# Optimization experiments

Hardware: AMD Instinct MI355X
Metric: run time of the kernel (lower is better)

## Reference

```python
import jax, jax.numpy as jnp
import numpy as np

B, T, D, H, O = 512, 256, 128, 256, 128

def _lin(x, W, b):
    # torch Linear: y = x @ W.T + b, W is [out, in]
    return x @ W.T + b

def _n2n(x):
    return jnp.nan_to_num(x, nan=0.0, posinf=0.0, neginf=0.0)

def _forward(x, x_mask, x_delta, noise,
             W_emb, b_emb, W_d1, b_d1, W_d2, b_d2, W_c, b_c,
             W_z, b_z, W_r, b_r, W_h, b_h, ln_g, ln_b, W_o, b_o):
    # input embedding
    x = _n2n(_lin(x, W_emb, b_emb))                       # [B,T,D]
    x_mean = jax.lax.stop_gradient(jnp.mean(x, axis=1))   # [B,D] (detach in torch)
    x_mean = _n2n(x_mean)
    # deltas, clamped (vectorized over T; decay MLP has no recurrence)
    d = jnp.clip(jnp.nan_to_num(x_delta, nan=0.0, posinf=100.0, neginf=0.0), 0.0, 100.0)
    gamma_x = jax.nn.sigmoid(_lin(jax.nn.relu(_lin(d, W_d1, b_d1)), W_d2, b_d2))  # [B,T,D]
    m = x_mask
    x_hat = m * x + (1.0 - m) * (gamma_x * x_mean[:, None, :])
    conf = jax.nn.sigmoid(_lin(jnp.concatenate([x_hat, d], axis=-1), W_c, b_c))   # [B,T,D]
    x_final = _n2n(x_hat * conf + noise * (1.0 - conf))
    # concat [x_final, m, d] is the time-varying part of gate inputs; nan_to_num
    xc = _n2n(jnp.concatenate([x_final, m, d], axis=-1))  # [B,T,3D]
    D3 = 3 * D
    # split gate weights into input-part and hidden-part; precompute input GEMMs
    zx = jnp.einsum('btk,hk->bth', xc, W_z[:, :D3]) + b_z  # [B,T,H]
    rx = jnp.einsum('btk,hk->bth', xc, W_r[:, :D3]) + b_r
    hx = jnp.einsum('btk,hk->bth', xc, W_h[:, :D3]) + b_h
    W_zh, W_rh, W_hh = W_z[:, D3:], W_r[:, D3:], W_h[:, D3:]

    def step(h, inp):
        zx_t, rx_t, hx_t = inp
        z = jax.nn.sigmoid(zx_t + h @ W_zh.T)
        r = jax.nn.sigmoid(rx_t + h @ W_rh.T)
        h_tilde = jnp.tanh(hx_t + (r * h) @ W_hh.T)
        h = _n2n((1.0 - z) * h + z * h_tilde)
        return h, None

    h0 = jnp.zeros((x.shape[0], H), dtype=x.dtype)
    h_last, _ = jax.lax.scan(step, h0, (zx.swapaxes(0, 1), rx.swapaxes(0, 1), hx.swapaxes(0, 1)))
    h_last = _n2n(h_last)
    # output head: LayerNorm(eps=1e-5) -> Dropout(eval: identity) -> Linear
    mu = jnp.mean(h_last, axis=-1, keepdims=True)
    var = jnp.mean((h_last - mu) ** 2, axis=-1, keepdims=True)
    ln = (h_last - mu) / jnp.sqrt(var + 1e-5) * ln_g + ln_b
    return _lin(ln, W_o, b_o)


def setup_inputs() -> dict:
    key = jax.random.key(0)
    ks = jax.random.split(key, 24)
    def W(k, o, i):
        s = 1.0 / np.sqrt(i)
        return jax.random.uniform(k, (o, i), jnp.float32, -s, s)
    def bvec(k, o, i):
        s = 1.0 / np.sqrt(i)
        return jax.random.uniform(k, (o,), jnp.float32, -s, s)
    D3H = 3 * D + H
    return {
        'x': jax.random.normal(ks[0], (B, T, D), jnp.float32),
        'x_mask': (jax.random.uniform(ks[1], (B, T, D)) < 0.8).astype(jnp.float32),
        'x_delta': jax.random.uniform(ks[2], (B, T, D), jnp.float32, 0.0, 10.0),
        'noise': jax.random.normal(ks[3], (B, T, D), jnp.float32),
        'W_emb': W(ks[4], D, D), 'b_emb': bvec(ks[5], D, D),
        'W_d1': W(ks[6], D, D), 'b_d1': bvec(ks[7], D, D),
        'W_d2': W(ks[8], D, D), 'b_d2': bvec(ks[9], D, D),
        'W_c': W(ks[10], D, 2 * D), 'b_c': bvec(ks[11], D, 2 * D),
        'W_z': W(ks[12], H, D3H), 'b_z': bvec(ks[13], H, D3H),
        'W_r': W(ks[14], H, D3H), 'b_r': bvec(ks[15], H, D3H),
        'W_h': W(ks[16], H, D3H), 'b_h': bvec(ks[17], H, D3H),
        'ln_g': jnp.ones((H,), jnp.float32), 'ln_b': jnp.zeros((H,), jnp.float32),
        'W_o': W(ks[18], O, H), 'b_o': bvec(ks[19], O, H),
    }


def reference(x, x_mask, x_delta, noise, W_emb, b_emb, W_d1, b_d1, W_d2, b_d2,
              W_c, b_c, W_z, b_z, W_r, b_r, W_h, b_h, ln_g, ln_b, W_o, b_o):
    return _forward(x, x_mask, x_delta, noise, W_emb, b_emb, W_d1, b_d1, W_d2, b_d2,
                    W_c, b_c, W_z, b_z, W_r, b_r, W_h, b_h, ln_g, ln_b, W_o, b_o)
```

## Files before the change

kernel.cpp:

```cpp
#include <hip/hip_runtime.h>
#include <hip/hip_fp16.h>
#include <math.h>

#define BB 512
#define TT 256
#define DD 128
#define HH 256
#define OO 128
#define KH 640
#define BT (BB*TT)

typedef unsigned int uint_t;
typedef _Float16 f16x8 __attribute__((ext_vector_type(8)));
typedef float f32x4 __attribute__((ext_vector_type(4)));

__device__ __forceinline__ float sigmoidf_(float x){ return 1.0f/(1.0f+__expf(-x)); }
__device__ __forceinline__ float tanhf_(float x){ float e = __expf(-2.0f*x); return 2.0f/(1.0f+e) - 1.0f; }
__device__ __forceinline__ float clipd_(float x){ return fminf(fmaxf(x, 0.f), 100.f); }

typedef _Float16 h2v __attribute__((ext_vector_type(2)));
__device__ __forceinline__ float d2(uint_t a, uint_t b, float c){
#if __has_builtin(__builtin_amdgcn_fdot2)
    return __builtin_amdgcn_fdot2(__builtin_bit_cast(h2v, a), __builtin_bit_cast(h2v, b), c, false);
#else
    __half2 ha = __builtin_bit_cast(__half2, a);
    __half2 hb = __builtin_bit_cast(__half2, b);
    return c + __half2float(ha.x)*__half2float(hb.x) + __half2float(ha.y)*__half2float(hb.y);
#endif
}
__device__ __forceinline__ uint_t pack2(float a, float b){
    __half2 h; h.x = __float2half(a); h.y = __float2half(b);
    return __builtin_bit_cast(uint_t, h);
}

static const size_t SZ_XC   = (size_t)BT*384*2;
static const size_t TAIL_SZ = 589824 + 393216 + 3072 + 262144 + 524288 + 32768*3 + 65536;

__global__ __launch_bounds__(128) void k_wprep(const float* __restrict__ Wz, const float* __restrict__ Wr,
                                               const float* __restrict__ Wh, const float* __restrict__ bz,
                                               const float* __restrict__ br, const float* __restrict__ bh,
                                               __half* __restrict__ Wcat, __half* __restrict__ Wrec,
                                               float* __restrict__ bcat){
    int gj = blockIdx.x; int j = gj & 255;
    const float* src  = (gj < 256 ? Wz : (gj < 512 ? Wr : Wh)) + (size_t)j*KH;
    const float* bsrc = (gj < 256 ? bz : (gj < 512 ? br : bh));
    for(int k=threadIdx.x; k<384; k+=128) Wcat[(size_t)gj*384 + k] = __float2half(src[k]);
    for(int k=threadIdx.x; k<256; k+=128) Wrec[(size_t)gj*256 + k] = __float2half(src[384+k]);
    if(threadIdx.x==0) bcat[gj] = bsrc[j];
}

__global__ __launch_bounds__(256) void k_cvt(const float* __restrict__ a, const float* __restrict__ b,
                                             const float* __restrict__ c, const float* __restrict__ d,
                                             __half* __restrict__ oa, __half* __restrict__ ob,
                                             __half* __restrict__ oc, __half* __restrict__ od){
    int i = blockIdx.x*256 + threadIdx.x;
    if(i < 16384){
        oa[i] = __float2half(a[i]);
        ob[i] = __float2half(b[i]);
        oc[i] = __float2half(c[i]);
    }
    od[i] = __float2half(d[i]);
}

__global__ __launch_bounds__(256,4) void k_embm(const float* __restrict__ x,
                                                const __half* __restrict__ Wh,
                                                const float* __restrict__ bias,
                                                __half* __restrict__ xc){
    __shared__ __align__(16) uint4 TxU[128*16];
    const int tid = threadIdx.x;
    const long row0 = (long)blockIdx.x*128;
    {
        const int srow = tid>>1, shalf = tid&1;
        const long gr = row0 + srow;
        const float4* gx = (const float4*)(x + gr*DD + shalf*64);
        #pragma unroll
        for(int u=0;u<8;++u){
            float4 a = gx[u*2], q = gx[u*2+1];
            uint4 pk;
            pk.x = pack2(a.x,a.y); pk.y = pack2(a.z,a.w);
            pk.z = pack2(q.x,q.y); pk.w = pack2(q.z,q.w);
            int unit = shalf*8 + u;
            TxU[srow*16 + (unit ^ (srow&7))] = pk;
        }
    }
    __syncthreads();
    const int wv = tid>>6, lane = tid&63, g = lane>>4, r16 = lane&15;
    const int wrow0 = wv*32;
    const uint4* WU = (const uint4*)Wh;
    f32x4 acc[2][8];
    #pragma unroll
    for(int i=0;i<2;++i)
        #pragma unroll
        for(int jj=0;jj<8;++jj) acc[i][jj] = (f32x4){0.f,0.f,0.f,0.f};
    #pragma unroll
    for(int ks=0;ks<4;++ks){
        f16x8 af[2], bf[8];
        #pragma unroll
        for(int mf=0;mf<2;++mf){
            int rr = wrow0 + mf*16 + r16;
            af[mf] = __builtin_bit_cast(f16x8, TxU[rr*16 + ((ks*4+g) ^ (rr&7))]);
        }
        #pragma unroll
        for(int nf=0;nf<8;++nf){
            int col = nf*16 + r16;
            bf[nf] = __builtin_bit_cast(f16x8, WU[col*16 + ks*4 + g]);
        }
        #pragma unroll
        for(int mf=0;mf<2;++mf)
            #pragma unroll
            for(int nf=0;nf<8;++nf)
                acc[mf][nf] = __builtin_amdgcn_mfma_f32_16x16x32_f16(af[mf], bf[nf], acc[mf][nf], 0,0,0);
    }
// ... 43 lines not shown
    const float* __restrict__ noise,
    const __half* __restrict__ Wd1h, const float* __restrict__ bd1,
    const __half* __restrict__ Wd2h, const float* __restrict__ bd2,
    const __half* __restrict__ Wch,  const float* __restrict__ bc,
    const float* __restrict__ xmean){
    __shared__ __align__(16) uint4 TdU[128*16];
    __shared__ __align__(16) uint4 TtU[128*16];
    __half* Tth = (__half*)TtU;
    const int tid = threadIdx.x;
    const long row0 = (long)blockIdx.x*128;
    const int b = (int)(row0 >> 8);

    {
        const int srow = tid>>1, shalf = tid&1;
        const long gr = row0 + srow;
        const float4* gd = (const float4*)(xdelta + gr*DD + shalf*64);
        const float4* gm = (const float4*)(xmask  + gr*DD + shalf*64);
        uint4* xcu = (uint4*)(xc + gr*384);
        #pragma unroll
        for(int u=0;u<8;++u){
            float4 a = gd[u*2], q = gd[u*2+1];
            uint4 pk;
            pk.x = pack2(clipd_(a.x), clipd_(a.y));
            pk.y = pack2(clipd_(a.z), clipd_(a.w));
            pk.z = pack2(clipd_(q.x), clipd_(q.y));
            pk.w = pack2(clipd_(q.z), clipd_(q.w));
            int unit = shalf*8 + u;
            TdU[srow*16 + (unit ^ (srow&7))] = pk;
            xcu[32 + unit] = pk;
        }
        #pragma unroll
        for(int u=0;u<8;++u){
            float4 a = gm[u*2], q = gm[u*2+1];
            uint4 pk;
            pk.x = pack2(a.x,a.y); pk.y = pack2(a.z,a.w);
            pk.z = pack2(q.x,q.y); pk.w = pack2(q.z,q.w);
            xcu[16 + shalf*8 + u] = pk;
        }
    }
    __syncthreads();

    const int wv = tid>>6, lane = tid&63, g = lane>>4, r16 = lane&15;
    const int wrow0 = wv*32;
    const uint4* W1U = (const uint4*)Wd1h;
    const uint4* W2U = (const uint4*)Wd2h;
    const uint4* WcU = (const uint4*)Wch;
    f32x4 acc[2][8];

    #pragma unroll
    for(int i=0;i<2;++i)
        #pragma unroll
        for(int jj=0;jj<8;++jj) acc[i][jj] = (f32x4){0.f,0.f,0.f,0.f};
    #pragma unroll
    for(int ks=0;ks<4;++ks){
        f16x8 af[2], bf[8];
        #pragma unroll
        for(int mf=0;mf<2;++mf){
            int rr = wrow0 + mf*16 + r16;
            af[mf] = __builtin_bit_cast(f16x8, TdU[rr*16 + ((ks*4+g) ^ (rr&7))]);
        }
        #pragma unroll
        for(int nf=0;nf<8;++nf){
            int col = nf*16 + r16;
            bf[nf] = __builtin_bit_cast(f16x8, W1U[col*16 + ks*4 + g]);
        }
        #pragma unroll
        for(int mf=0;mf<2;++mf)
            #pragma unroll
            for(int nf=0;nf<8;++nf)
                acc[mf][nf] = __builtin_amdgcn_mfma_f32_16x16x32_f16(af[mf], bf[nf], acc[mf][nf], 0,0,0);
    }
    #pragma unroll
    for(int nf=0;nf<8;++nf){
        int col = nf*16 + r16;
        float bb = bd1[col];
        int u = col>>3, cl = col&7;
        #pragma unroll
        for(int mf=0;mf<2;++mf){
            int rowb = wrow0 + mf*16 + g*4;
            f32x4 v = acc[mf][nf];
            #pragma unroll
            for(int e=0;e<4;++e){
                int rr = rowb + e;
                float t = v[e] + bb; t = t > 0.f ? t : 0.f;
                Tth[(rr*16 + (u ^ (rr&7)))*8 + cl] = __float2half(t);
            }
        }
    }

    #pragma unroll
    for(int i=0;i<2;++i)
        #pragma unroll
        for(int jj=0;jj<8;++jj) acc[i][jj] = (f32x4){0.f,0.f,0.f,0.f};
    #pragma unroll
    for(int ks=0;ks<4;++ks){
        f16x8 af[2], bf[8];
        #pragma unroll
        for(int mf=0;mf<2;++mf){
            int rr = wrow0 + mf*16 + r16;
            af[mf] = __builtin_bit_cast(f16x8, TtU[rr*16 + ((ks*4+g) ^ (rr&7))]);
        }
        #pragma unroll
        for(int nf=0;nf<8;++nf){
            int col = nf*16 + r16;
            bf[nf] = __builtin_bit_cast(f16x8, W2U[col*16 + ks*4 + g]);
        }
        #pragma unroll
        for(int mf=0;mf<2;++mf)
            #pragma unroll
            for(int nf=0;nf<8;++nf)
                acc[mf][nf] = __builtin_amdgcn_mfma_f32_16x16x32_f16(af[mf], bf[nf], acc[mf][nf], 0,0,0);
    }

    #pragma unroll
    for(int nf=0;nf<8;++nf){
        int col = nf*16 + r16;
        float b2 = bd2[col];
        float xm = xmean[b*DD + col];
        int u = col>>3, cl = col&7;
        #pragma unroll
        for(int mf=0;mf<2;++mf){
            int rowb = wrow0 + mf*16 + g*4;
            f32x4 v = acc[mf][nf];
            #pragma unroll
            for(int e=0;e<4;++e){
                int rr = rowb + e;
                long grow = row0 + rr;
                float m  = xmask[grow*DD + col];
                float x1 = __half2float(xc[grow*384 + col]);
                float gmm = sigmoidf_(v[e] + b2);
                float xh = m*x1 + (1.f-m)*gmm*xm;
                Tth[(rr*16 + (u ^ (rr&7)))*8 + cl] = __float2half(xh);
            }
        }
    }

    #pragma unroll
    for(int i=0;i<2;++i)
        #pragma unroll
        for(int jj=0;jj<8;++jj) acc[i][jj] = (f32x4){0.f,0.f,0.f,0.f};
    #pragma unroll
    for(int ks=0;ks<4;++ks){
        f16x8 af[2], bf[8];
        #pragma unroll
        for(int mf=0;mf<2;++mf){
            int rr = wrow0 + mf*16 + r16;
            af[mf] = __builtin_bit_cast(f16x8, TtU[rr*16 + ((ks*4+g) ^ (rr&7))]);
        }
        #pragma unroll
        for(int nf=0;nf<8;++nf){
            int col = nf*16 + r16;
            bf[nf] = __builtin_bit_cast(f16x8, WcU[col*32 + ks*4 + g]);
        }
        #pragma unroll
        for(int mf=0;mf<2;++mf)
            #pragma unroll
            for(int nf=0;nf<8;++nf)
                acc[mf][nf] = __builtin_amdgcn_mfma_f32_16x16x32_f16(af[mf], bf[nf], acc[mf][nf], 0,0,0);
    }
    #pragma unroll
    for(int ks=0;ks<4;++ks){
        f16x8 af[2], bf[8];
        #pragma unroll
        for(int mf=0;mf<2;++mf){
            int rr = wrow0 + mf*16 + r16;
            af[mf] = __builtin_bit_cast(f16x8, TdU[rr*16 + ((ks*4+g) ^ (rr&7))]);
        }
        #pragma unroll
        for(int nf=0;nf<8;++nf){
            int col = nf*16 + r16;
            bf[nf] = __builtin_bit_cast(f16x8, WcU[col*32 + 16 + ks*4 + g]);
        }
        #pragma unroll
        for(int mf=0;mf<2;++mf)
            #pragma unroll
            for(int nf=0;nf<8;++nf)
                acc[mf][nf] = __builtin_amdgcn_mfma_f32_16x16x32_f16(af[mf], bf[nf], acc[mf][nf], 0,0,0);
    }

    #pragma unroll
    for(int nf=0;nf<8;++nf){
        int col = nf*16 + r16;
        float bcc = bc[col];
        int u = col>>3, cl = col&7;
        #pragma unroll
        for(int mf=0;mf<2;++mf){
            int rowb = wrow0 + mf*16 + g*4;
            f32x4 v = acc[mf][nf];
            #pragma unroll
            for(int e=0;e<4;++e){
                int rr = rowb + e;
                long grow = row0 + rr;
                float conf = sigmoidf_(v[e] + bcc);
                float xh = __half2float(Tth[(rr*16 + (u ^ (rr&7)))*8 + cl]);
                float nz = noise[grow*DD + col];
                xc[grow*384 + col] = __float2half(xh*conf + nz*(1.f-conf));
            }
        }
    }
}

__global__ __launch_bounds__(256) void k_projm(const __half* __restrict__ xc,
                                               const __half* __restrict__ Wcat,
                                               const float* __restrict__ bcat,
                                               __half* __restrict__ px,
                                               int lTc, int chunk){
    __shared__ __align__(16) __half As[128*64];
    __shared__ __align__(16) __half Bs[128*64];
    const int tid = threadIdx.x;
    const int rblk = blockIdx.x * 128;
    const int ct0  = blockIdx.y * 128;
    const int mTc = (1<<lTc) - 1;

    const int row = tid >> 1;
    const int hf  = tid & 1;
    const int ar  = rblk + row;
    const long grow = ((long)(ar >> lTc))*TT + ((long)chunk << lTc) + (ar & mTc);
    const uint4* gA = (const uint4*)(xc + grow*384);
    const uint4* gB = (const uint4*)(Wcat + (size_t)(ct0 + row)*384);
    uint4* AsU = (uint4*)As;
    uint4* BsU = (uint4*)Bs;

    const int wv = tid >> 6;
    const int wm = wv >> 1, wn = wv & 1;
    const int l  = tid & 63;
    const int g  = l >> 4, r16 = l & 15;

    f32x4 acc[4][4];
    #pragma unroll
    for(int i=0;i<4;++i)
        #pragma unroll
        for(int jj=0;jj<4;++jj) acc[i][jj] = (f32x4){0.f,0.f,0.f,0.f};

    for(int bk=0; bk<6; ++bk){
        uint4 av[4], bv[4];
        #pragma unroll
        for(int u=0;u<4;++u){ av[u] = gA[bk*8 + hf*4 + u]; bv[u] = gB[bk*8 + hf*4 + u]; }
        if(bk) __syncthreads();
        #pragma unroll
        for(int u=0;u<4;++u){
            int uu = hf*4 + u;
            AsU[row*8 + (uu ^ (row&7))] = av[u];
            BsU[row*8 + (uu ^ (row&7))] = bv[u];
        }
        __syncthreads();
        #pragma unroll
        for(int ks=0;ks<2;++ks){
            f16x8 af[4], bf[4];
            #pragma unroll
            for(int mf=0;mf<4;++mf){
                int rr = wm*64 + mf*16 + r16;
                af[mf] = __builtin_bit_cast(f16x8, AsU[rr*8 + ((ks*4+g) ^ (rr&7))]);
            }
            #pragma unroll
            for(int nf=0;nf<4;++nf){
                int rr = wn*64 + nf*16 + r16;
                bf[nf] = __builtin_bit_cast(f16x8, BsU[rr*8 + ((ks*4+g) ^ (rr&7))]);
            }
            #pragma unroll
            for(int mf=0;mf<4;++mf)
                #pragma unroll
                for(int nf=0;nf<4;++nf)
                    acc[mf][nf] = __builtin_amdgcn_mfma_f32_16x16x32_f16(af[mf], bf[nf], acc[mf][nf], 0,0,0);
        }
    }
    #pragma unroll
    for(int nf=0; nf<4; ++nf){
        int col = ct0 + wn*64 + nf*16 + r16;
        float bb = bcat[col];
        #pragma unroll
        for(int mf=0; mf<4; ++mf){
            int r0 = rblk + wm*64 + mf*16 + g*4;
            f32x4 v = acc[mf][nf];
            #pragma unroll
            for(int e=0;e<4;++e)
                px[(size_t)(r0+e)*768 + col] = __float2half(v[e] + bb);
        }
    }
}

__global__ __launch_bounds__(512,2) void k_gruc(const __half* __restrict__ pxc,
                                                const __half* __restrict__ Wrec,
                                                float* __restrict__ hstate,
                                                int Tc, int init){
    __shared__ __align__(16) __half h16[2][256];
    __shared__ __align__(16) __half rh16[2][256];
    __shared__ __align__(16) uint_t pxs[2][768];
    const int t  = threadIdx.x;
    const int j  = t >> 1;
    const int kh = t & 1;
    const long b0 = (long)blockIdx.x*2;
    const uint_t* Wr32 = (const uint_t*)Wrec;

    uint_t wz[64], wr[64], wh[64];
    #pragma unroll
    for(int q=0;q<64;++q){
        wz[q] = Wr32[(size_t)(      j)*128 + kh*64 + q];
        wr[q] = Wr32[(size_t)(256 + j)*128 + kh*64 + q];
        wh[q] = Wr32[(size_t)(512 + j)*128 + kh*64 + q];
    }

    const uint_t* px32 = (const uint_t*)pxc;
    auto ldpx = [&](int tl, int f)->uint_t{
        int row = (f >= 384); int off = f - row*384;
        return px32[((size_t)(b0+row)*Tc + tl)*384 + off];
    };

    float hreg0, hreg1;
    if(init){ hreg0 = 0.f; hreg1 = 0.f; }
    else    { hreg0 = hstate[(b0+0)*HH + j]; hreg1 = hstate[(b0+1)*HH + j]; }
    if(kh==0){ h16[0][j] = __float2half(hreg0); h16[1][j] = __float2half(hreg1); }
    pxs[0][t] = ldpx(0, t);
    if(t < 256) pxs[0][t+512] = ldpx(0, t+512);
    __syncthreads();

    const uint_t* h0p = ((const uint_t*)&h16[0][0]) + kh*64;
    const uint_t* h1p = ((const uint_t*)&h16[1][0]) + kh*64;
    const uint_t* r0p = ((const uint_t*)&rh16[0][0]) + kh*64;
    const uint_t* r1p = ((const uint_t*)&rh16[1][0]) + kh*64;

    for(int s=0; s<Tc; ++s){
        const int cur = s & 1;
        uint_t nf0 = 0, nf1 = 0;
        if(s < Tc-1){ nf0 = ldpx(s+1, t); if(t < 256) nf1 = ldpx(s+1, t+512); }

        const __half* pxcur = (const __half*)pxs[cur];
        float az0=0.f, az1=0.f, ar0=0.f, ar1=0.f;
        #pragma unroll
        for(int q=0;q<64;q+=4){
            uint4 hv0 = *(const uint4*)(h0p + q);
            uint4 hv1 = *(const uint4*)(h1p + q);
            az0=d2(wz[q+0],hv0.x,az0); ar0=d2(wr[q+0],hv0.x,ar0); az1=d2(wz[q+0],hv1.x,az1); ar1=d2(wr[q+0],hv1.x,ar1);
            az0=d2(wz[q+1],hv0.y,az0); ar0=d2(wr[q+1],hv0.y,ar0); az1=d2(wz[q+1],hv1.y,az1); ar1=d2(wr[q+1],hv1.y,ar1);
            az0=d2(wz[q+2],hv0.z,az0); ar0=d2(wr[q+2],hv0.z,ar0); az1=d2(wz[q+2],hv1.z,az1); ar1=d2(wr[q+2],hv1.z,ar1);
            az0=d2(wz[q+3],hv0.w,az0); ar0=d2(wr[q+3],hv0.w,ar0); az1=d2(wz[q+3],hv1.w,az1); ar1=d2(wr[q+3],hv1.w,ar1);
        }
        az0 += __shfl_xor(az0,1); az1 += __shfl_xor(az1,1);
        ar0 += __shfl_xor(ar0,1); ar1 += __shfl_xor(ar1,1);
        float z0 = sigmoidf_(__half2float(pxcur[        j]) + az0);
        float z1 = sigmoidf_(__half2float(pxcur[768   + j]) + az1);
        float r0 = sigmoidf_(__half2float(pxcur[256   + j]) + ar0);
        float r1 = sigmoidf_(__half2float(pxcur[768+256+j]) + ar1);
        if(kh==0){
            rh16[0][j] = __float2half(r0*hreg0);
            rh16[1][j] = __float2half(r1*hreg1);
        }
        __syncthreads();
        float ah0=0.f, ah1=0.f;
        #pragma unroll
        for(int q=0;q<64;q+=4){
            uint4 rv0 = *(const uint4*)(r0p + q);
            uint4 rv1 = *(const uint4*)(r1p + q);
            ah0=d2(wh[q+0],rv0.x,ah0); ah1=d2(wh[q+0],rv1.x,ah1);
            ah0=d2(wh[q+1],rv0.y,ah0); ah1=d2(wh[q+1],rv1.y,ah1);
            ah0=d2(wh[q+2],rv0.z,ah0); ah1=d2(wh[q+2],rv1.z,ah1);
            ah0=d2(wh[q+3],rv0.w,ah0); ah1=d2(wh[q+3],rv1.w,ah1);
        }
        ah0 += __shfl_xor(ah0,1); ah1 += __shfl_xor(ah1,1);
        float ht0 = tanhf_(__half2float(pxcur[512    + j]) + ah0);
        float ht1 = tanhf_(__half2float(pxcur[768+512+j]) + ah1);
        hreg0 = (1.f - z0)*hreg0 + z0*ht0;
        hreg1 = (1.f - z1)*hreg1 + z1*ht1;
        if(kh==0){
            h16[0][j] = __float2half(hreg0);
            h16[1][j] = __float2half(hreg1);
        }
        if(s < Tc-1){
            pxs[cur^1][t] = nf0;
            if(t < 256) pxs[cur^1][t+512] = nf1;
        }
        __syncthreads();
    }
    if(kh==0){
        hstate[(b0+0)*HH + j] = hreg0;
        hstate[(b0+1)*HH + j] = hreg1;
    }
}

__global__ __launch_bounds__(256) void k_lnout(const float* __restrict__ hbuf,
    const float* __restrict__ lng, const float* __restrict__ lnb,
    const float* __restrict__ Wo, const float* __restrict__ bo,
    float* __restrict__ out){
    __shared__ __align__(16) float ln_s[HH];
    __shared__ float red[8];
    const int b = blockIdx.x, j = threadIdx.x;
    const float v = hbuf[(long)b*HH + j];
    float s = v, ss = v*v;
    const int lane = j & 63, w = j >> 6;
    for(int off=32; off>0; off>>=1){
        s  += __shfl_down(s,  off);
        ss += __shfl_down(ss, off);
    }
    if(lane == 0){ red[w] = s; red[4+w] = ss; }
    __syncthreads();
    float tot  = red[0]+red[1]+red[2]+red[3];
    float tot2 = red[4]+red[5]+red[6]+red[7];
    float mu  = tot  * (1.0f/HH);
    float var = tot2 * (1.0f/HH) - mu*mu;
    float rstd = rsqrtf(var + 1e-5f);
    ln_s[j] = (v - mu)*rstd*lng[j] + lnb[j];
    __syncthreads();
    if(j < OO){
        float acc = bo[j];
        const float4* w4 = (const float4*)(Wo + j*HH);
        const float4* l4 = (const float4*)ln_s;
        for(int k4=0;k4<HH/4;++k4){
            float4 wv = w4[k4], c = l4[k4];
            acc += wv.x*c.x + wv.y*c.y + wv.z*c.z + wv.w*c.w;
        }
        out[(long)b*OO + j] = acc;
    }
}


__global__ __launch_bounds__(128) void k_emb_o(const float* __restrict__ x,
                                               const float* __restrict__ W,
                                               const float* __restrict__ bias,
                                               float* __restrict__ x1){
    __shared__ __align__(16) float xs[8][DD];
    const int j = threadIdx.x;
    const long row0 = (long)blockIdx.x * 32;
    const float bj = bias[j];
    const float4* W4 = (const float4*)(W + j*DD);
    for(int g=0; g<4; ++g){
        const long rbase = row0 + g*8;
        for(int r=0;r<8;++r) xs[r][j] = x[(rbase+r)*DD + j];
        __syncthreads();
        float acc[8];
        #pragma unroll
        for(int r=0;r<8;++r) acc[r] = bj;
        for(int k4=0;k4<DD/4;++k4){
            float4 w = W4[k4];
            #pragma unroll
            for(int r=0;r<8;++r){
                float4 c = ((const float4*)xs[r])[k4];
                acc[r] += c.x*w.x + c.y*w.y + c.z*w.z + c.w*w.w;
            }
        }
        for(int r=0;r<8;++r) x1[(rbase+r)*DD + j] = acc[r];
        __syncthreads();
    }
}

__global__ __launch_bounds__(128) void k_mean_o(const float* __restrict__ x1,
                                                float* __restrict__ xmean){
    const int j = threadIdx.x;
    const int b = blockIdx.x;
    const float* p = x1 + (long)b*TT*DD + j;
    float s = 0.f;
    for(int t=0;t<TT;++t) s += p[(long)t*DD];
    xmean[b*DD + j] = s * (1.0f/TT);
}

__global__ __launch_bounds__(128) void k_gate_o(float* __restrict__ xf,
    const float* __restrict__ xmask, const float* __restrict__ xdelta,
    const float* __restrict__ noise,
    const float* __restrict__ Wd1, const float* __restrict__ bd1,
    const float* __restrict__ Wd2, const float* __restrict__ bd2,
// ... 115 lines not shown
        float ah = bhj;
        for(int k4=0;k4<96;++k4){
            float4 wh = Wh4[k4];
            float4 v = cb[k4];
            ah += v.x*wh.x + v.y*wh.y + v.z*wh.z + v.w*wh.w;
        }
        const float4* rp = (const float4*)rh[bl];
        for(int k4=0;k4<64;++k4){
            float4 wh = Wh4[96 + k4];
            float4 v = rp[k4];
            ah += v.x*wh.x + v.y*wh.y + v.z*wh.z + v.w*wh.w;
        }
        float ht = tanhf(ah);
        float hold = xcs[bl][384 + j];
        float hn = (1.f - z)*hold + z*ht;
        xcs[bl][384 + j] = hn;
        __syncthreads();
    }
    hout[(bbase + bl)*HH + j] = xcs[bl][384 + j];
}


extern "C" void kernel_launch(void* const* d_in, const int* in_sizes, int n_in,
                              void* d_out, int out_size, void* d_ws, size_t ws_size,
                              hipStream_t stream){
    const float* x      = (const float*)d_in[0];
    const float* xmask  = (const float*)d_in[1];
    const float* xdelta = (const float*)d_in[2];
    const float* noise  = (const float*)d_in[3];
    const float* W_emb  = (const float*)d_in[4];
    const float* b_emb  = (const float*)d_in[5];
    const float* W_d1   = (const float*)d_in[6];
    const float* b_d1   = (const float*)d_in[7];
    const float* W_d2   = (const float*)d_in[8];
    const float* b_d2   = (const float*)d_in[9];
    const float* W_c    = (const float*)d_in[10];
    const float* b_c    = (const float*)d_in[11];
    const float* W_z    = (const float*)d_in[12];
    const float* b_z    = (const float*)d_in[13];
    const float* W_r    = (const float*)d_in[14];
    const float* b_r    = (const float*)d_in[15];
    const float* W_h    = (const float*)d_in[16];
    const float* b_h    = (const float*)d_in[17];
    const float* ln_g   = (const float*)d_in[18];
    const float* ln_b   = (const float*)d_in[19];
    const float* W_o    = (const float*)d_in[20];
    const float* b_o    = (const float*)d_in[21];
    float* out = (float*)d_out;
    char* ws = (char*)d_ws;

    int Tc = 0, lTc = 0;
    {
        const int cand[3]  = {128, 64, 32};
        const int lcand[3] = {7, 6, 5};
        for(int i=0;i<3;++i){
            size_t need = SZ_XC + (size_t)cand[i]*786432 + TAIL_SZ;
            if(ws_size >= need){ Tc = cand[i]; lTc = lcand[i]; break; }
        }
    }

    if(Tc > 0){
        __half* xc    = (__half*)(ws);
        char*   p     = ws + SZ_XC;
        __half* pxc   = (__half*)p;              p += (size_t)Tc*786432;
        __half* Wcat  = (__half*)p;              p += 589824;
        __half* Wrec  = (__half*)p;              p += 393216;
        float*  bcat  = (float*)p;               p += 3072;
        float*  xmean = (float*)p;               p += 262144;
        float*  hstate= (float*)p;               p += 524288;
        __half* Wembh = (__half*)p;              p += 32768;
        __half* Wd1h  = (__half*)p;              p += 32768;
        __half* Wd2h  = (__half*)p;              p += 32768;
        __half* Wch   = (__half*)p;

        k_wprep<<<dim3(768),   dim3(128), 0, stream>>>(W_z,W_r,W_h,b_z,b_r,b_h, Wcat, Wrec, bcat);
        k_cvt  <<<dim3(128),   dim3(256), 0, stream>>>(W_emb, W_d1, W_d2, W_c, Wembh, Wd1h, Wd2h, Wch);
        k_embm <<<dim3(BT/128),dim3(256), 0, stream>>>(x, Wembh, b_emb, xc);
        k_meanv<<<dim3(BB),    dim3(256), 0, stream>>>(xc, xmean);
        k_gatem<<<dim3(BT/128),dim3(256), 0, stream>>>(xc, xmask, xdelta, noise,
                                                       Wd1h,b_d1,Wd2h,b_d2,Wch,b_c, xmean);
        const int nchunk = TT / Tc;
        for(int c=0; c<nchunk; ++c){
            k_projm<<<dim3(BB*Tc/128, 6), dim3(256), 0, stream>>>(xc, Wcat, bcat, pxc, lTc, c);
            k_gruc <<<dim3(BB/2), dim3(512), 0, stream>>>(pxc, Wrec, hstate, Tc, c==0 ? 1 : 0);
        }
        k_lnout<<<dim3(BB), dim3(256), 0, stream>>>(hstate, ln_g, ln_b, W_o, b_o, out);
    } else {
        float* xf    = (float*)ws;
        float* xmean = (float*)(ws + (size_t)BT*DD*4);
        float* hbuf  = (float*)(ws + (size_t)BT*DD*4 + (size_t)BB*DD*4);
        k_emb_o  <<<dim3(BT/32), dim3(128), 0, stream>>>(x, W_emb, b_emb, xf);
        k_mean_o <<<dim3(BB),    dim3(128), 0, stream>>>(xf, xmean);
        k_gate_o <<<dim3(BT/32), dim3(128), 0, stream>>>(xf, xmask, xdelta, noise,
                                                         W_d1,b_d1,W_d2,b_d2,W_c,b_c, xmean);
        k_gru_o  <<<dim3(BB/4),  dim3(1024),0, stream>>>(xf, xmask, xdelta,
                                                         W_z,b_z,W_r,b_r,W_h,b_h, hbuf);
        k_lnout  <<<dim3(BB),    dim3(256), 0, stream>>>(hbuf, ln_g, ln_b, W_o, b_o, out);
    }
}
```

Baseline: 1.388 ms.

## Split GRU recurrent dot products four ways with padded LDS layout for h

Reworks the recurrent GRU kernel so each thread covers two hidden units across a quarter of the K dimension, instead of one unit across half of K. Weights are held in uint4 vectors and partial sums are reduced with two shuffle-xor steps. The fp16 hidden state in LDS gets a padded layout (72-word stride per 64 entries) so the four K-slices read from different banks. The intent is to cut LDS bank conflicts and load count per step, at the cost of extra shuffles and more accumulators.

```diff
diff --git a/kernel.cpp b/kernel.cpp
--- a/kernel.cpp
+++ b/kernel.cpp
@@ -237,8 +237,8 @@
             #pragma unroll
             for(int e=0;e<4;++e){
                 int rr = rowb + e;
-                float t = v[e] + bb; t = t > 0.f ? t : 0.f;
-                Tth[(rr*16 + (u ^ (rr&7)))*8 + cl] = __float2half(t);
+                float tt = v[e] + bb; tt = tt > 0.f ? tt : 0.f;
+                Tth[(rr*16 + (u ^ (rr&7)))*8 + cl] = __float2half(tt);
             }
         }
     }
@@ -438,21 +438,24 @@
                                                 const __half* __restrict__ Wrec,
                                                 float* __restrict__ hstate,
                                                 int Tc, int init){
-    __shared__ __align__(16) __half h16[2][256];
-    __shared__ __align__(16) __half rh16[2][256];
+    __shared__ __align__(16) uint_t hU[288];
+    __shared__ __align__(16) uint_t rhU[288];
     __shared__ __align__(16) uint_t pxs[2][768];
     const int t  = threadIdx.x;
-    const int j  = t >> 1;
-    const int kh = t & 1;
+    const int ks = t & 3;
+    const int jj = t >> 2;
     const long b0 = (long)blockIdx.x*2;
-    const uint_t* Wr32 = (const uint_t*)Wrec;
-
-    uint_t wz[64], wr[64], wh[64];
-    #pragma unroll
-    for(int q=0;q<64;++q){
-        wz[q] = Wr32[(size_t)(      j)*128 + kh*64 + q];
-        wr[q] = Wr32[(size_t)(256 + j)*128 + kh*64 + q];
-        wh[q] = Wr32[(size_t)(512 + j)*128 + kh*64 + q];
+    const uint4* Wr4 = (const uint4*)Wrec;
+
+    uint4 wz0[8], wz1[8], wr0[8], wr1[8], wh0[8], wh1[8];
+    #pragma unroll
+    for(int q=0;q<8;++q){
+        wz0[q] = Wr4[(size_t)(      jj     )*32 + ks*8 + q];
+        wz1[q] = Wr4[(size_t)(      jj+128 )*32 + ks*8 + q];
+        wr0[q] = Wr4[(size_t)(256 + jj     )*32 + ks*8 + q];
+        wr1[q] = Wr4[(size_t)(256 + jj+128 )*32 + ks*8 + q];
+        wh0[q] = Wr4[(size_t)(512 + jj     )*32 + ks*8 + q];
+        wh1[q] = Wr4[(size_t)(512 + jj+128 )*32 + ks*8 + q];
     }
 
     const uint_t* px32 = (const uint_t*)pxc;
@@ -461,18 +464,33 @@
         return px32[((size_t)(b0+row)*Tc + tl)*384 + off];
     };
 
-    float hreg0, hreg1;
-    if(init){ hreg0 = 0.f; hreg1 = 0.f; }
-    else    { hreg0 = hstate[(b0+0)*HH + j]; hreg1 = hstate[(b0+1)*HH + j]; }
-    if(kh==0){ h16[0][j] = __float2half(hreg0); h16[1][j] = __float2half(hreg1); }
+    const int ho0 = ((jj>>6)*72) + (jj&63);
+    const int ho1 = ho0 + 144;
+    __half* hh  = (__half*)hU;
+    __half* rhh = (__half*)rhU;
+
+    float h00,h01,h10,h11;
+    if(init){ h00=0.f; h01=0.f; h10=0.f; h11=0.f; }
+    else{
+        h00 = hstate[(b0+0)*HH + jj];
+        h01 = hstate[(b0+0)*HH + jj+128];
+        h10 = hstate[(b0+1)*HH + jj];
+        h11 = hstate[(b0+1)*HH + jj+128];
+    }
+    if(ks==0){
+        hh[      ho0] = __float2half(h00);
+        hh[      ho1] = __float2half(h01);
+        hh[288 + ho0] = __float2half(h10);
+        hh[288 + ho1] = __float2half(h11);
+    }
     pxs[0][t] = ldpx(0, t);
     if(t < 256) pxs[0][t+512] = ldpx(0, t+512);
     __syncthreads();
 
-    const uint_t* h0p = ((const uint_t*)&h16[0][0]) + kh*64;
-    const uint_t* h1p = ((const uint_t*)&h16[1][0]) + kh*64;
-    const uint_t* r0p = ((const uint_t*)&rh16[0][0]) + kh*64;
-    const uint_t* r1p = ((const uint_t*)&rh16[1][0]) + kh*64;
+    const uint4* h0p = ((const uint4*)hU)       + ks*9;
+    const uint4* h1p = ((const uint4*)hU)  + 36 + ks*9;
+    const uint4* r0p = ((const uint4*)rhU)      + ks*9;
+    const uint4* r1p = ((const uint4*)rhU) + 36 + ks*9;
 
     for(int s=0; s<Tc; ++s){
         const int cur = s & 1;
@@ -480,45 +498,74 @@
         if(s < Tc-1){ nf0 = ldpx(s+1, t); if(t < 256) nf1 = ldpx(s+1, t+512); }
 
         const __half* pxcur = (const __half*)pxs[cur];
-        float az0=0.f, az1=0.f, ar0=0.f, ar1=0.f;
-        #pragma unroll
-        for(int q=0;q<64;q+=4){
-            uint4 hv0 = *(const uint4*)(h0p + q);
-            uint4 hv1 = *(const uint4*)(h1p + q);
-            az0=d2(wz[q+0],hv0.x,az0); ar0=d2(wr[q+0],hv0.x,ar0); az1=d2(wz[q+0],hv1.x,az1); ar1=d2(wr[q+0],hv1.x,ar1);
-            az0=d2(wz[q+1],hv0.y,az0); ar0=d2(wr[q+1],hv0.y,ar0); az1=d2(wz[q+1],hv1.y,az1); ar1=d2(wr[q+1],hv1.y,ar1);
-            az0=d2(wz[q+2],hv0.z,az0); ar0=d2(wr[q+2],hv0.z,ar0); az1=d2(wz[q+2],hv1.z,az1); ar1=d2(wr[q+2],hv1.z,ar1);
-            az0=d2(wz[q+3],hv0.w,az0); ar0=d2(wr[q+3],hv0.w,ar0); az1=d2(wz[q+3],hv1.w,az1); ar1=d2(wr[q+3],hv1.w,ar1);
-        }
-        az0 += __shfl_xor(az0,1); az1 += __shfl_xor(az1,1);
-        ar0 += __shfl_xor(ar0,1); ar1 += __shfl_xor(ar1,1);
-        float z0 = sigmoidf_(__half2float(pxcur[        j]) + az0);
-        float z1 = sigmoidf_(__half2float(pxcur[768   + j]) + az1);
-        float r0 = sigmoidf_(__half2float(pxcur[256   + j]) + ar0);
-        float r1 = sigmoidf_(__half2float(pxcur[768+256+j]) + ar1);
-        if(kh==0){
-            rh16[0][j] = __float2half(r0*hreg0);
-            rh16[1][j] = __float2half(r1*hreg1);
-        }
-        __syncthreads();
-        float ah0=0.f, ah1=0.f;
-        #pragma unroll
-        for(int q=0;q<64;q+=4){
-            uint4 rv0 = *(const uint4*)(r0p + q);
-            uint4 rv1 = *(const uint4*)(r1p + q);
-            ah0=d2(wh[q+0],rv0.x,ah0); ah1=d2(wh[q+0],rv1.x,ah1);
-            ah0=d2(wh[q+1],rv0.y,ah0); ah1=d2(wh[q+1],rv1.y,ah1);
-            ah0=d2(wh[q+2],rv0.z,ah0); ah1=d2(wh[q+2],rv1.z,ah1);
-            ah0=d2(wh[q+3],rv0.w,ah0); ah1=d2(wh[q+3],rv1.w,ah1);
-        }
-        ah0 += __shfl_xor(ah0,1); ah1 += __shfl_xor(ah1,1);
-        float ht0 = tanhf_(__half2float(pxcur[512    + j]) + ah0);
-        float ht1 = tanhf_(__half2float(pxcur[768+512+j]) + ah1);
-        hreg0 = (1.f - z0)*hreg0 + z0*ht0;
-        hreg1 = (1.f - z1)*hreg1 + z1*ht1;
-        if(kh==0){
-            h16[0][j] = __float2half(hreg0);
-            h16[1][j] = __float2half(hreg1);
+        float az00=0.f,az01=0.f,az10=0.f,az11=0.f;
+        float ar00=0.f,ar01=0.f,ar10=0.f,ar11=0.f;
+        #pragma unroll
+        for(int it=0; it<8; ++it){
+            uint4 hv0 = h0p[it], hv1 = h1p[it];
+            uint4 a = wz0[it], b = wz1[it], c = wr0[it], d = wr1[it];
+            az00=d2(a.x,hv0.x,az00); az00=d2(a.y,hv0.y,az00); az00=d2(a.z,hv0.z,az00); az00=d2(a.w,hv0.w,az00);
+            az01=d2(b.x,hv0.x,az01); az01=d2(b.y,hv0.y,az01); az01=d2(b.z,hv0.z,az01); az01=d2(b.w,hv0.w,az01);
+            az10=d2(a.x,hv1.x,az10); az10=d2(a.y,hv1.y,az10); az10=d2(a.z,hv1.z,az10); az10=d2(a.w,hv1.w,az10);
+            az11=d2(b.x,hv1.x,az11); az11=d2(b.y,hv1.y,az11); az11=d2(b.z,hv1.z,az11); az11=d2(b.w,hv1.w,az11);
+            ar00=d2(c.x,hv0.x,ar00); ar00=d2(c.y,hv0.y,ar00); ar00=d2(c.z,hv0.z,ar00); ar00=d2(c.w,hv0.w,ar00);
+            ar01=d2(d.x,hv0.x,ar01); ar01=d2(d.y,hv0.y,ar01); ar01=d2(d.z,hv0.z,ar01); ar01=d2(d.w,hv0.w,ar01);
+            ar10=d2(c.x,hv1.x,ar10); ar10=d2(c.y,hv1.y,ar10); ar10=d2(c.z,hv1.z,ar10); ar10=d2(c.w,hv1.w,ar10);
+            ar11=d2(d.x,hv1.x,ar11); ar11=d2(d.y,hv1.y,ar11); ar11=d2(d.z,hv1.z,ar11); ar11=d2(d.w,hv1.w,ar11);
+        }
+        az00 += __shfl_xor(az00,1); az00 += __shfl_xor(az00,2);
+        az01 += __shfl_xor(az01,1); az01 += __shfl_xor(az01,2);
+        az10 += __shfl_xor(az10,1); az10 += __shfl_xor(az10,2);
+        az11 += __shfl_xor(az11,1); az11 += __shfl_xor(az11,2);
+        ar00 += __shfl_xor(ar00,1); ar00 += __shfl_xor(ar00,2);
+        ar01 += __shfl_xor(ar01,1); ar01 += __shfl_xor(ar01,2);
+        ar10 += __shfl_xor(ar10,1); ar10 += __shfl_xor(ar10,2);
+        ar11 += __shfl_xor(ar11,1); ar11 += __shfl_xor(ar11,2);
+
+        float z00 = sigmoidf_(__half2float(pxcur[      jj    ]) + az00);
+        float z01 = sigmoidf_(__half2float(pxcur[      jj+128]) + az01);
+        float z10 = sigmoidf_(__half2float(pxcur[768 + jj    ]) + az10);
+        float z11 = sigmoidf_(__half2float(pxcur[768 + jj+128]) + az11);
+        float r00 = sigmoidf_(__half2float(pxcur[256 + jj    ]) + ar00);
+        float r01 = sigmoidf_(__half2float(pxcur[256 + jj+128]) + ar01);
+        float r10 = sigmoidf_(__half2float(pxcur[768+256+jj    ]) + ar10);
+        float r11 = sigmoidf_(__half2float(pxcur[768+256+jj+128]) + ar11);
+        if(ks==0){
+            rhh[      ho0] = __float2half(r00*h00);
+            rhh[      ho1] = __float2half(r01*h01);
+            rhh[288 + ho0] = __float2half(r10*h10);
+            rhh[288 + ho1] = __float2half(r11*h11);
+        }
+        __syncthreads();
+
+        float ah00=0.f,ah01=0.f,ah10=0.f,ah11=0.f;
+        #pragma unroll
+        for(int it=0; it<8; ++it){
+            uint4 rv0 = r0p[it], rv1 = r1p[it];
+            uint4 a = wh0[it], b = wh1[it];
+            ah00=d2(a.x,rv0.x,ah00); ah00=d2(a.y,rv0.y,ah00); ah00=d2(a.z,rv0.z,ah00); ah00=d2(a.w,rv0.w,ah00);
+            ah01=d2(b.x,rv0.x,ah01); ah01=d2(b.y,rv0.y,ah01); ah01=d2(b.z,rv0.z,ah01); ah01=d2(b.w,rv0.w,ah01);
+            ah10=d2(a.x,rv1.x,ah10); ah10=d2(a.y,rv1.y,ah10); ah10=d2(a.z,rv1.z,ah10); ah10=d2(a.w,rv1.w,ah10);
+            ah11=d2(b.x,rv1.x,ah11); ah11=d2(b.y,rv1.y,ah11); ah11=d2(b.z,rv1.z,ah11); ah11=d2(b.w,rv1.w,ah11);
+        }
+        ah00 += __shfl_xor(ah00,1); ah00 += __shfl_xor(ah00,2);
+        ah01 += __shfl_xor(ah01,1); ah01 += __shfl_xor(ah01,2);
+        ah10 += __shfl_xor(ah10,1); ah10 += __shfl_xor(ah10,2);
+        ah11 += __shfl_xor(ah11,1); ah11 += __shfl_xor(ah11,2);
+
+        float ht00 = tanhf_(__half2float(pxcur[512 + jj    ]) + ah00);
+        float ht01 = tanhf_(__half2float(pxcur[512 + jj+128]) + ah01);
+        float ht10 = tanhf_(__half2float(pxcur[768+512+jj    ]) + ah10);
+        float ht11 = tanhf_(__half2float(pxcur[768+512+jj+128]) + ah11);
+        h00 = (1.f - z00)*h00 + z00*ht00;
+        h01 = (1.f - z01)*h01 + z01*ht01;
+        h10 = (1.f - z10)*h10 + z10*ht10;
+        h11 = (1.f - z11)*h11 + z11*ht11;
+        if(ks==0){
+            hh[      ho0] = __float2half(h00);
+            hh[      ho1] = __float2half(h01);
+            hh[288 + ho0] = __float2half(h10);
+            hh[288 + ho1] = __float2half(h11);
         }
         if(s < Tc-1){
             pxs[cur^1][t] = nf0;
@@ -526,9 +573,11 @@
         }
         __syncthreads();
     }
-    if(kh==0){
-        hstate[(b0+0)*HH + j] = hreg0;
-        hstate[(b0+1)*HH + j] = hreg1;
+    if(ks==0){
+        hstate[(b0+0)*HH + jj]     = h00;
+        hstate[(b0+0)*HH + jj+128] = h01;
+        hstate[(b0+1)*HH + jj]     = h10;
+        hstate[(b0+1)*HH + jj+128] = h11;
     }
 }
 
```

After: 1.481 ms. +6.7%, slower.

## Batch GRU recurrence over 16 rows per block using MFMA

Applied to the files above, without the earlier changes.

Replaces the per-thread fdot2 GRU recurrence, which handled 2 batch rows per block, with an MFMA-based kernel that handles 16 batch rows per block. The z/r and candidate matvecs become 16x16x32 f16 MFMAs. To match, the input projection now writes its output in a batch-interleaved transposed layout so each step's inputs load as contiguous vectors. The aim is to cut per-step instruction latency in the serial recurrence. The trade-off is only 32 blocks on the GPU, an extra barrier per step, and the candidate weights re-read from global memory every step.

```diff
diff --git a/kernel.cpp b/kernel.cpp
--- a/kernel.cpp
+++ b/kernel.cpp
@@ -18,16 +18,6 @@
 __device__ __forceinline__ float tanhf_(float x){ float e = __expf(-2.0f*x); return 2.0f/(1.0f+e) - 1.0f; }
 __device__ __forceinline__ float clipd_(float x){ return fminf(fmaxf(x, 0.f), 100.f); }
 
-typedef _Float16 h2v __attribute__((ext_vector_type(2)));
-__device__ __forceinline__ float d2(uint_t a, uint_t b, float c){
-#if __has_builtin(__builtin_amdgcn_fdot2)
-    return __builtin_amdgcn_fdot2(__builtin_bit_cast(h2v, a), __builtin_bit_cast(h2v, b), c, false);
-#else
-    __half2 ha = __builtin_bit_cast(__half2, a);
-    __half2 hb = __builtin_bit_cast(__half2, b);
-    return c + __half2float(ha.x)*__half2float(hb.x) + __half2float(ha.y)*__half2float(hb.y);
-#endif
-}
 __device__ __forceinline__ uint_t pack2(float a, float b){
     __half2 h; h.x = __float2half(a); h.y = __float2half(b);
     return __builtin_bit_cast(uint_t, h);
@@ -237,8 +227,8 @@
             #pragma unroll
             for(int e=0;e<4;++e){
                 int rr = rowb + e;
-                float t = v[e] + bb; t = t > 0.f ? t : 0.f;
-                Tth[(rr*16 + (u ^ (rr&7)))*8 + cl] = __float2half(t);
+                float tt = v[e] + bb; tt = tt > 0.f ? tt : 0.f;
+                Tth[(rr*16 + (u ^ (rr&7)))*8 + cl] = __float2half(tt);
             }
         }
     }
@@ -366,6 +356,7 @@
     const int rblk = blockIdx.x * 128;
     const int ct0  = blockIdx.y * 128;
     const int mTc = (1<<lTc) - 1;
+    const int Tcv = 1<<lTc;
 
     const int row = tid >> 1;
     const int hf  = tid & 1;
@@ -428,107 +419,184 @@
             int r0 = rblk + wm*64 + mf*16 + g*4;
             f32x4 v = acc[mf][nf];
             #pragma unroll
-            for(int e=0;e<4;++e)
-                px[(size_t)(r0+e)*768 + col] = __float2half(v[e] + bb);
-        }
-    }
-}
-
-__global__ __launch_bounds__(512,2) void k_gruc(const __half* __restrict__ pxc,
+            for(int e=0;e<4;++e){
+                int are = r0 + e;
+                int brow = are >> lTc;
+                int tl   = are & mTc;
+                px[((size_t)((brow>>4)*Tcv + tl))*12288 + (size_t)col*16 + (brow&15)] = __float2half(v[e] + bb);
+            }
+        }
+    }
+}
+
+__global__ __launch_bounds__(512,2) void k_grum(const __half* __restrict__ pxT,
                                                 const __half* __restrict__ Wrec,
                                                 float* __restrict__ hstate,
                                                 int Tc, int init){
-    __shared__ __align__(16) __half h16[2][256];
-    __shared__ __align__(16) __half rh16[2][256];
-    __shared__ __align__(16) uint_t pxs[2][768];
-    const int t  = threadIdx.x;
-    const int j  = t >> 1;
-    const int kh = t & 1;
-    const long b0 = (long)blockIdx.x*2;
-    const uint_t* Wr32 = (const uint_t*)Wrec;
-
-    uint_t wz[64], wr[64], wh[64];
-    #pragma unroll
-    for(int q=0;q<64;++q){
-        wz[q] = Wr32[(size_t)(      j)*128 + kh*64 + q];
-        wr[q] = Wr32[(size_t)(256 + j)*128 + kh*64 + q];
-        wh[q] = Wr32[(size_t)(512 + j)*128 + kh*64 + q];
-    }
-
-    const uint_t* px32 = (const uint_t*)pxc;
-    auto ldpx = [&](int tl, int f)->uint_t{
-        int row = (f >= 384); int off = f - row*384;
-        return px32[((size_t)(b0+row)*Tc + tl)*384 + off];
-    };
-
-    float hreg0, hreg1;
-    if(init){ hreg0 = 0.f; hreg1 = 0.f; }
-    else    { hreg0 = hstate[(b0+0)*HH + j]; hreg1 = hstate[(b0+1)*HH + j]; }
-    if(kh==0){ h16[0][j] = __float2half(hreg0); h16[1][j] = __float2half(hreg1); }
-    pxs[0][t] = ldpx(0, t);
-    if(t < 256) pxs[0][t+512] = ldpx(0, t+512);
+    __shared__ __align__(16) uint4 pxL[2][2304];
+    __shared__ __align__(16) uint4 hAu[16*33];
+    __shared__ __align__(16) uint4 rhAu[16*33];
+    __shared__ __align__(16) uint2 zrB[512*6];
+    __shared__ float hF[16*265];
+
+    const int tid = threadIdx.x;
+    const int w   = tid >> 6;
+    const int l   = tid & 63;
+    const int g   = l >> 4;
+    const int r16 = l & 15;
+    const long b0 = (long)blockIdx.x * 16;
+    const uint4* WrU = (const uint4*)Wrec;
+    __half* hAh = (__half*)hAu;
+    __half* zrH = (__half*)zrB;
+
+    uint4 wb1[4][8];
+    #pragma unroll
+    for(int tc=0;tc<4;++tc){
+        int col = w*64 + tc*16 + r16;
+        #pragma unroll
+        for(int kf=0;kf<8;++kf)
+            wb1[tc][kf] = WrU[(size_t)col*32 + kf*4 + g];
+    }
+    const int col2a = w*32 + r16;
+    const int col2b = w*32 + 16 + r16;
+
+    {
+        int brow = tid >> 5;
+        int c8 = (tid & 31) * 8;
+        uint4 pk;
+        float hv[8];
+        if(init){
+            #pragma unroll
+            for(int e=0;e<8;++e) hv[e] = 0.f;
+        } else {
+            const float* hs = hstate + (b0 + brow)*HH + c8;
+            #pragma unroll
+            for(int e=0;e<8;++e) hv[e] = hs[e];
+        }
+        pk.x = pack2(hv[0],hv[1]); pk.y = pack2(hv[2],hv[3]);
+        pk.z = pack2(hv[4],hv[5]); pk.w = pack2(hv[6],hv[7]);
+        hAu[brow*33 + (c8>>3)] = pk;
+        #pragma unroll
+        for(int e=0;e<8;++e) hF[brow*265 + c8 + e] = hv[e];
+    }
+    const uint4* pxg = (const uint4*)pxT + (size_t)blockIdx.x * Tc * 1536;
+    {
+        #pragma unroll
+        for(int q=0;q<3;++q){
+            int i = tid + q*512;
+            uint4 v = pxg[i];
+            pxL[0][(i>>1)*3 + (i&1)] = v;
+        }
+    }
     __syncthreads();
 
-    const uint_t* h0p = ((const uint_t*)&h16[0][0]) + kh*64;
-    const uint_t* h1p = ((const uint_t*)&h16[1][0]) + kh*64;
-    const uint_t* r0p = ((const uint_t*)&rh16[0][0]) + kh*64;
-    const uint_t* r1p = ((const uint_t*)&rh16[1][0]) + kh*64;
-
+    int cur = 0;
     for(int s=0; s<Tc; ++s){
-        const int cur = s & 1;
-        uint_t nf0 = 0, nf1 = 0;
-        if(s < Tc-1){ nf0 = ldpx(s+1, t); if(t < 256) nf1 = ldpx(s+1, t+512); }
-
-        const __half* pxcur = (const __half*)pxs[cur];
-        float az0=0.f, az1=0.f, ar0=0.f, ar1=0.f;
-        #pragma unroll
-        for(int q=0;q<64;q+=4){
-            uint4 hv0 = *(const uint4*)(h0p + q);
-            uint4 hv1 = *(const uint4*)(h1p + q);
-            az0=d2(wz[q+0],hv0.x,az0); ar0=d2(wr[q+0],hv0.x,ar0); az1=d2(wz[q+0],hv1.x,az1); ar1=d2(wr[q+0],hv1.x,ar1);
-            az0=d2(wz[q+1],hv0.y,az0); ar0=d2(wr[q+1],hv0.y,ar0); az1=d2(wz[q+1],hv1.y,az1); ar1=d2(wr[q+1],hv1.y,ar1);
-            az0=d2(wz[q+2],hv0.z,az0); ar0=d2(wr[q+2],hv0.z,ar0); az1=d2(wz[q+2],hv1.z,az1); ar1=d2(wr[q+2],hv1.z,ar1);
-            az0=d2(wz[q+3],hv0.w,az0); ar0=d2(wr[q+3],hv0.w,ar0); az1=d2(wz[q+3],hv1.w,az1); ar1=d2(wr[q+3],hv1.w,ar1);
-        }
-        az0 += __shfl_xor(az0,1); az1 += __shfl_xor(az1,1);
-        ar0 += __shfl_xor(ar0,1); ar1 += __shfl_xor(ar1,1);
-        float z0 = sigmoidf_(__half2float(pxcur[        j]) + az0);
-        float z1 = sigmoidf_(__half2float(pxcur[768   + j]) + az1);
-        float r0 = sigmoidf_(__half2float(pxcur[256   + j]) + ar0);
-        float r1 = sigmoidf_(__half2float(pxcur[768+256+j]) + ar1);
-        if(kh==0){
-            rh16[0][j] = __float2half(r0*hreg0);
-            rh16[1][j] = __float2half(r1*hreg1);
-        }
-        __syncthreads();
-        float ah0=0.f, ah1=0.f;
-        #pragma unroll
-        for(int q=0;q<64;q+=4){
-            uint4 rv0 = *(const uint4*)(r0p + q);
-            uint4 rv1 = *(const uint4*)(r1p + q);
-            ah0=d2(wh[q+0],rv0.x,ah0); ah1=d2(wh[q+0],rv1.x,ah1);
-            ah0=d2(wh[q+1],rv0.y,ah0); ah1=d2(wh[q+1],rv1.y,ah1);
-            ah0=d2(wh[q+2],rv0.z,ah0); ah1=d2(wh[q+2],rv1.z,ah1);
-            ah0=d2(wh[q+3],rv0.w,ah0); ah1=d2(wh[q+3],rv1.w,ah1);
-        }
-        ah0 += __shfl_xor(ah0,1); ah1 += __shfl_xor(ah1,1);
-        float ht0 = tanhf_(__half2float(pxcur[512    + j]) + ah0);
-        float ht1 = tanhf_(__half2float(pxcur[768+512+j]) + ah1);
-        hreg0 = (1.f - z0)*hreg0 + z0*ht0;
-        hreg1 = (1.f - z1)*hreg1 + z1*ht1;
-        if(kh==0){
-            h16[0][j] = __float2half(hreg0);
-            h16[1][j] = __float2half(hreg1);
-        }
+        uint4 nx0, nx1, nx2;
         if(s < Tc-1){
-            pxs[cur^1][t] = nf0;
-            if(t < 256) pxs[cur^1][t+512] = nf1;
-        }
-        __syncthreads();
-    }
-    if(kh==0){
-        hstate[(b0+0)*HH + j] = hreg0;
-        hstate[(b0+1)*HH + j] = hreg1;
+            const uint4* pg = pxg + (size_t)(s+1)*1536;
+            nx0 = pg[tid]; nx1 = pg[tid+512]; nx2 = pg[tid+1024];
+        }
+        uint4 wb2a[8], wb2b[8];
+        #pragma unroll
+        for(int kf=0;kf<8;++kf){
+            wb2a[kf] = WrU[(size_t)(512+col2a)*32 + kf*4 + g];
+            wb2b[kf] = WrU[(size_t)(512+col2b)*32 + kf*4 + g];
+        }
+        const uint2* pxc2 = (const uint2*)pxL[cur];
+
+        f32x4 acc[4];
+        #pragma unroll
+        for(int tc=0;tc<4;++tc){
+            int col = w*64 + tc*16 + r16;
+            uint2 pv = pxc2[col*6 + g];
+            __half2 p0 = __builtin_bit_cast(__half2, pv.x);
+            __half2 p1 = __builtin_bit_cast(__half2, pv.y);
+            acc[tc] = (f32x4){ __half2float(p0.x), __half2float(p0.y),
+                               __half2float(p1.x), __half2float(p1.y) };
+        }
+        #pragma unroll
+        for(int kf=0;kf<8;++kf){
+            f16x8 af = __builtin_bit_cast(f16x8, hAu[r16*33 + kf*4 + g]);
+            #pragma unroll
+            for(int tc=0;tc<4;++tc)
+                acc[tc] = __builtin_amdgcn_mfma_f32_16x16x32_f16(af, __builtin_bit_cast(f16x8, wb1[tc][kf]), acc[tc], 0,0,0);
+        }
+        #pragma unroll
+        for(int tc=0;tc<4;++tc){
+            int col = w*64 + tc*16 + r16;
+            uint2 zz;
+            zz.x = pack2(sigmoidf_(acc[tc][0]), sigmoidf_(acc[tc][1]));
+            zz.y = pack2(sigmoidf_(acc[tc][2]), sigmoidf_(acc[tc][3]));
+            zrB[col*6 + g] = zz;
+        }
+        __syncthreads();
+
+        {
+            int brow = tid>>5, c8 = (tid&31)*8;
+            uint4 hv = hAu[brow*33 + (c8>>3)];
+            const __half* hp = (const __half*)&hv;
+            float rf[8];
+            #pragma unroll
+            for(int e=0;e<8;++e)
+                rf[e] = __half2float(zrH[(256 + c8 + e)*24 + brow]) * __half2float(hp[e]);
+            uint4 rv;
+            rv.x = pack2(rf[0],rf[1]); rv.y = pack2(rf[2],rf[3]);
+            rv.z = pack2(rf[4],rf[5]); rv.w = pack2(rf[6],rf[7]);
+            rhAu[brow*33 + (c8>>3)] = rv;
+        }
+        __syncthreads();
+
+        f32x4 acc2[2];
+        {
+            uint2 pva = pxc2[(512+col2a)*6 + g];
+            uint2 pvb = pxc2[(512+col2b)*6 + g];
+            __half2 a0 = __builtin_bit_cast(__half2, pva.x);
+            __half2 a1 = __builtin_bit_cast(__half2, pva.y);
+            __half2 b0h = __builtin_bit_cast(__half2, pvb.x);
+            __half2 b1h = __builtin_bit_cast(__half2, pvb.y);
+            acc2[0] = (f32x4){ __half2float(a0.x), __half2float(a0.y),
+                               __half2float(a1.x), __half2float(a1.y) };
+            acc2[1] = (f32x4){ __half2float(b0h.x), __half2float(b0h.y),
+                               __half2float(b1h.x), __half2float(b1h.y) };
+        }
+        #pragma unroll
+        for(int kf=0;kf<8;++kf){
+            f16x8 af = __builtin_bit_cast(f16x8, rhAu[r16*33 + kf*4 + g]);
+            acc2[0] = __builtin_amdgcn_mfma_f32_16x16x32_f16(af, __builtin_bit_cast(f16x8, wb2a[kf]), acc2[0], 0,0,0);
+            acc2[1] = __builtin_amdgcn_mfma_f32_16x16x32_f16(af, __builtin_bit_cast(f16x8, wb2b[kf]), acc2[1], 0,0,0);
+        }
+        #pragma unroll
+        for(int tc=0;tc<2;++tc){
+            int col = (tc==0) ? col2a : col2b;
+            uint2 zz = zrB[col*6 + g];
+            __half2 z0 = __builtin_bit_cast(__half2, zz.x);
+            __half2 z1 = __builtin_bit_cast(__half2, zz.y);
+            float zf[4] = { __half2float(z0.x), __half2float(z0.y),
+                            __half2float(z1.x), __half2float(z1.y) };
+            #pragma unroll
+            for(int e=0;e<4;++e){
+                int brow = g*4 + e;
+                float ho = hF[brow*265 + col];
+                float ht = tanhf_(acc2[tc][e]);
+                float hn = (1.f - zf[e])*ho + zf[e]*ht;
+                hF[brow*265 + col] = hn;
+                hAh[brow*264 + col] = __float2half(hn);
+            }
+        }
+        if(s < Tc-1){
+            { int i=tid;      pxL[cur^1][(i>>1)*3+(i&1)] = nx0; }
+            { int i=tid+512;  pxL[cur^1][(i>>1)*3+(i&1)] = nx1; }
+            { int i=tid+1024; pxL[cur^1][(i>>1)*3+(i&1)] = nx2; }
+            cur ^= 1;
+        }
+        __syncthreads();
+    }
+    {
+        int brow = tid>>5, c8 = (tid&31)*8;
+        float* hs = hstate + (b0+brow)*HH + c8;
+        #pragma unroll
+        for(int e=0;e<8;++e) hs[e] = hF[brow*265 + c8 + e];
     }
 }
 
@@ -810,7 +878,7 @@
         const int nchunk = TT / Tc;
         for(int c=0; c<nchunk; ++c){
             k_projm<<<dim3(BB*Tc/128, 6), dim3(256), 0, stream>>>(xc, Wcat, bcat, pxc, lTc, c);
-            k_gruc <<<dim3(BB/2), dim3(512), 0, stream>>>(pxc, Wrec, hstate, Tc, c==0 ? 1 : 0);
+            k_grum <<<dim3(32), dim3(512), 0, stream>>>(pxc, Wrec, hstate, Tc, c==0 ? 1 : 0);
         }
         k_lnout<<<dim3(BB), dim3(256), 0, stream>>>(hstate, ln_g, ln_b, W_o, b_o, out);
     } else {
```

New measurement: 2.315 ms. 66.8% more time.
